# Kernel optimization log

Hardware: AMD Instinct MI355X
Metric: run time of the kernel (lower is better)

Reference implementation:

```python
import jax, jax.numpy as jnp
import numpy as np


def fake_quant(w, bits):
    # Symmetric per-tensor fake quantization with straight-through estimator.
    qmax = 2.0 ** (bits - 1) - 1.0
    scale = jnp.max(jnp.abs(w)) / qmax
    wq = jnp.clip(jnp.round(w / scale), -qmax, qmax) * scale
    return w + jax.lax.stop_gradient(wq - w)


def setup_inputs() -> dict:
    key = jax.random.key(0)
    k = jax.random.split(key, 5)
    B, S, D, H = 64, 196, 768, 3072
    x = jax.random.normal(k[0], (B, S, D), dtype=jnp.float32)
    w1 = jax.random.normal(k[1], (H, D), dtype=jnp.float32) * (1.0 / np.sqrt(D))
    b1 = jax.random.normal(k[2], (H,), dtype=jnp.float32) * 0.01
    w2 = jax.random.normal(k[3], (D, H), dtype=jnp.float32) * (1.0 / np.sqrt(H))
    b2 = jax.random.normal(k[4], (D,), dtype=jnp.float32) * 0.01
    return {"x": x, "w1": w1, "b1": b1, "w2": w2, "b2": b2, "bits": 8}


def reference(x, w1, b1, w2, b2, bits):
    # fc1 (fake-quant weight) -> ReLU -> fc2 (fake-quant weight)
    w1q = fake_quant(w1, bits)
    w2q = fake_quant(w2, bits)
    h = jnp.einsum('bsd,hd->bsh', x, w1q) + b1   # [B,S,3072]
    h = jax.nn.relu(h)
    out = jnp.einsum('bsh,dh->bsd', h, w2q) + b2  # [B,S,768]
    return out
```

## Files before the change

kernel.cpp:

```cpp
#include <hip/hip_runtime.h>
#include <hip/hip_bf16.h>
#include <stdint.h>

typedef __attribute__((ext_vector_type(8))) short bf16x8;
typedef __attribute__((ext_vector_type(4))) float f32x4;

__device__ __forceinline__ unsigned short f2bf(float f) {
  __hip_bfloat16 h = __float2bfloat16(f);
  return *reinterpret_cast<unsigned short*>(&h);
}

__global__ void prep_kernel(const float* __restrict__ w1, const float* __restrict__ w2,
                            const float* __restrict__ x, int n4w, int n4x,
                            unsigned int* __restrict__ pmax,
                            unsigned short* __restrict__ ox) {
  if (blockIdx.y == 2) {
    const float4* x4 = reinterpret_cast<const float4*>(x);
    ushort4* o4 = reinterpret_cast<ushort4*>(ox);
    for (int i = blockIdx.x * blockDim.x + threadIdx.x; i < n4x;
         i += gridDim.x * blockDim.x) {
      float4 v = x4[i];
      o4[i] = make_ushort4(f2bf(v.x), f2bf(v.y), f2bf(v.z), f2bf(v.w));
    }
    return;
  }
  const float* w = blockIdx.y ? w2 : w1;
  __shared__ unsigned int red[256];
  unsigned int m = 0u;
  const uint4* w4 = reinterpret_cast<const uint4*>(w);
  for (int i = blockIdx.x * blockDim.x + threadIdx.x; i < n4w;
       i += gridDim.x * blockDim.x) {
    uint4 v = w4[i];
    m = max(m, v.x & 0x7fffffffu);
    m = max(m, v.y & 0x7fffffffu);
    m = max(m, v.z & 0x7fffffffu);
    m = max(m, v.w & 0x7fffffffu);
  }
  red[threadIdx.x] = m;
  __syncthreads();
  for (int s = 128; s > 0; s >>= 1) {
    if ((int)threadIdx.x < s)
      red[threadIdx.x] = max(red[threadIdx.x], red[threadIdx.x + s]);
    __syncthreads();
  }
  if (threadIdx.x == 0) pmax[blockIdx.y * 512 + blockIdx.x] = red[0];
}

__global__ void quant2_kernel(const float* __restrict__ w1, const float* __restrict__ w2,
                              int n4, const unsigned int* __restrict__ pmax,
                              const int* __restrict__ bits,
                              unsigned short* __restrict__ o1, unsigned short* __restrict__ o2) {
  __shared__ unsigned int red[256];
  const unsigned int* p = pmax + blockIdx.y * 512;
  red[threadIdx.x] = max(p[threadIdx.x], p[threadIdx.x + 256]);
  __syncthreads();
  for (int s = 128; s > 0; s >>= 1) {
    if ((int)threadIdx.x < s)
      red[threadIdx.x] = max(red[threadIdx.x], red[threadIdx.x + s]);
    __syncthreads();
  }
  const float qmax = (float)((1 << (*bits - 1)) - 1);
  const float scale = __uint_as_float(red[0]) / qmax;

  const float* w = blockIdx.y ? w2 : w1;
  unsigned short* o = blockIdx.y ? o2 : o1;
  const float4* w4 = reinterpret_cast<const float4*>(w);
  ushort4* o4 = reinterpret_cast<ushort4*>(o);
  for (int i = blockIdx.x * blockDim.x + threadIdx.x; i < n4;
       i += gridDim.x * blockDim.x) {
    float4 v = w4[i];
    float a = fminf(fmaxf(rintf(v.x / scale), -qmax), qmax) * scale;
    float b = fminf(fmaxf(rintf(v.y / scale), -qmax), qmax) * scale;
    float c = fminf(fmaxf(rintf(v.z / scale), -qmax), qmax) * scale;
    float d = fminf(fmaxf(rintf(v.w / scale), -qmax), qmax) * scale;
    o4[i] = make_ushort4(f2bf(a), f2bf(b), f2bf(c), f2bf(d));
  }
}

template<bool PRIO, bool RELU, bool BF16_OUT>
__global__ __launch_bounds__(256, 4)
void gemm_bt32(const unsigned short* __restrict__ A,
               const unsigned short* __restrict__ B,
               const float* __restrict__ bias,
               void* __restrict__ Cout,
               int M, int N, int K, int gx) {
  constexpr int BK = 32, MF = 4;
  __shared__ __attribute__((aligned(16))) unsigned short As[2][128 * BK];
  __shared__ __attribute__((aligned(16))) unsigned short Bs[2][128 * BK];

  const int nwg = gridDim.x;
  const int orig = blockIdx.x;
  const int q = nwg >> 3, r = nwg & 7;
  const int xcd = orig & 7, cidx = orig >> 3;
  const int wgid = (xcd < r ? xcd * (q + 1) : r * (q + 1) + (xcd - r) * q) + cidx;
  const int bx = wgid % gx;
  const int by = wgid / gx;

  const int tid = threadIdx.x;
  const int lane = tid & 63;
  const int wave = tid >> 6;
  const int wr = wave >> 1;
  const int wc = wave & 1;
  const long brow = (long)by * 128;
  const long bcol = (long)bx * 128;

  f32x4 acc[MF][4] = {};

  const int srow = lane >> 2;
  const int gslot = ((lane & 3) ^ ((lane >> 3) & 3)) * 8;
  const int fr = lane & 15;
  const int fs = lane >> 4;

  auto stage = [&](int k0, int b) {
#pragma unroll
    for (int it = 0; it < 2; ++it) {
      const int c = it * 4 + wave;
      const unsigned short* ga = A + (brow + c * 16 + srow) * (long)K + k0 + gslot;
      __builtin_amdgcn_global_load_lds(
          (const __attribute__((address_space(1))) void*)ga,
          (__attribute__((address_space(3))) void*)(&As[b][c * 512]), 16, 0, 0);
    }
#pragma unroll
    for (int it = 0; it < 2; ++it) {
      const int c = it * 4 + wave;
      const unsigned short* gb = B + (bcol + c * 16 + srow) * (long)K + k0 + gslot;
      __builtin_amdgcn_global_load_lds(
          (const __attribute__((address_space(1))) void*)gb,
          (__attribute__((address_space(3))) void*)(&Bs[b][c * 512]), 16, 0, 0);
    }
  };

  const int nt = K / BK;
  stage(0, 0);
  stage(BK, 1);

  for (int t = 0; t < nt; ++t) {
    const int b = t & 1;
    if (t < nt - 1) asm volatile("s_waitcnt vmcnt(4)" ::: "memory");
    else            asm volatile("s_waitcnt vmcnt(0)" ::: "memory");
    __builtin_amdgcn_s_barrier();

    const unsigned short* as = &As[b][0];
    const unsigned short* bs = &Bs[b][0];
    bf16x8 a[MF], bb[4];
#pragma unroll
    for (int m = 0; m < MF; ++m) {
      const int row = wr * 64 + m * 16 + fr;
      a[m] = *reinterpret_cast<const bf16x8*>(as + row * BK + ((fs ^ ((row >> 1) & 3)) * 8));
    }
#pragma unroll
    for (int n = 0; n < 4; ++n) {
      const int row = wc * 64 + n * 16 + fr;
      bb[n] = *reinterpret_cast<const bf16x8*>(bs + row * BK + ((fs ^ ((row >> 1) & 3)) * 8));
    }
    if (PRIO) __builtin_amdgcn_s_setprio(1);
#pragma unroll
    for (int m = 0; m < MF; ++m)
#pragma unroll
      for (int n = 0; n < 4; ++n)
        acc[m][n] = __builtin_amdgcn_mfma_f32_16x16x32_bf16(a[m], bb[n], acc[m][n], 0, 0, 0);
    if (PRIO) __builtin_amdgcn_s_setprio(0);

    asm volatile("s_waitcnt lgkmcnt(0)" ::: "memory");
    __builtin_amdgcn_sched_barrier(0);
    __builtin_amdgcn_s_barrier();
    if (t + 2 < nt) stage((t + 2) * BK, b);
  }

  const int fq = lane >> 4;
#pragma unroll
  for (int n = 0; n < 4; ++n) {
    const long col = bcol + wc * 64 + n * 16 + fr;
    const float bv = bias[col];
#pragma unroll
    for (int m = 0; m < MF; ++m) {
#pragma unroll
      for (int rr = 0; rr < 4; ++rr) {
        const long row = brow + wr * 64 + m * 16 + fq * 4 + rr;
        float v = acc[m][n][rr] + bv;
        if (RELU) v = fmaxf(v, 0.0f);
        if (BF16_OUT)
          ((unsigned short*)Cout)[row * N + col] = f2bf(v);
        else
          ((float*)Cout)[row * N + col] = v;
      }
    }
  }
}

template<int BM, bool PRIO, bool RELU, bool BF16_OUT>
__global__ __launch_bounds__(256)
void gemm_bt(const unsigned short* __restrict__ A, const unsigned short* __restrict__ B,
             const float* __restrict__ bias, void* __restrict__ Cout,
             int M, int N, int K, int gx) {
  constexpr int BK = 64;
  constexpr int MF = BM / 32;
  __shared__ __attribute__((aligned(16))) unsigned short As[2][BM * BK];
  __shared__ __attribute__((aligned(16))) unsigned short Bs[2][128 * BK];

  const int nwg = gridDim.x;
  const int orig = blockIdx.x;
  const int q = nwg >> 3, r = nwg & 7;
  const int xcd = orig & 7, cidx = orig >> 3;
  const int wgid = (xcd < r ? xcd * (q + 1) : r * (q + 1) + (xcd - r) * q) + cidx;
  const int bx = wgid % gx;
  const int by = wgid / gx;

  const int tid = threadIdx.x;
  const int lane = tid & 63;
  const int wave = tid >> 6;
  const int wr = wave >> 1;
  const int wc = wave & 1;
  const long brow = (long)by * BM;
  const long bcol = (long)bx * 128;

  f32x4 acc[MF][4] = {};

  const int srow = lane >> 3;
  const int gslot = ((lane & 7) ^ (lane >> 3)) * 8;
  const int fr = lane & 15;
  const int fs = lane >> 4;

  auto stage = [&](int k0, int b) {
#pragma unroll
    for (int it = 0; it < BM / 32; ++it) {
      const int c = it * 4 + wave;
      const unsigned short* ga = A + (brow + c * 8 + srow) * (long)K + k0 + gslot;
      __builtin_amdgcn_global_load_lds(
          (const __attribute__((address_space(1))) void*)ga,
          (__attribute__((address_space(3))) void*)(&As[b][c * 512]), 16, 0, 0);
    }
#pragma unroll
    for (int it = 0; it < 4; ++it) {
      const int c = it * 4 + wave;
      const unsigned short* gb = B + (bcol + c * 8 + srow) * (long)K + k0 + gslot;
      __builtin_amdgcn_global_load_lds(
          (const __attribute__((address_space(1))) void*)gb,
          (__attribute__((address_space(3))) void*)(&Bs[b][c * 512]), 16, 0, 0);
    }
  };

  const int nt = K / BK;
  stage(0, 0);
  stage(BK, 1);

  for (int t = 0; t < nt; ++t) {
    const int b = t & 1;
    if (t < nt - 1) {
      if constexpr (BM == 128) asm volatile("s_waitcnt vmcnt(8)" ::: "memory");
      else                     asm volatile("s_waitcnt vmcnt(6)" ::: "memory");
    } else {
      asm volatile("s_waitcnt vmcnt(0)" ::: "memory");
    }
    __builtin_amdgcn_s_barrier();

    const unsigned short* as = &As[b][0];
    const unsigned short* bs = &Bs[b][0];
#pragma unroll
    for (int kk = 0; kk < 2; ++kk) {
      const int s = kk * 4 + fs;
      bf16x8 a[MF], bb[4];
#pragma unroll
      for (int m = 0; m < MF; ++m) {
        const int row = wr * (MF * 16) + m * 16 + fr;
        a[m] = *reinterpret_cast<const bf16x8*>(as + row * BK + ((s ^ (row & 7)) * 8));
      }
#pragma unroll
      for (int n = 0; n < 4; ++n) {
        const int row = wc * 64 + n * 16 + fr;
        bb[n] = *reinterpret_cast<const bf16x8*>(bs + row * BK + ((s ^ (row & 7)) * 8));
      }
      if (PRIO) __builtin_amdgcn_s_setprio(1);
#pragma unroll
      for (int m = 0; m < MF; ++m)
#pragma unroll
        for (int n = 0; n < 4; ++n)
          acc[m][n] = __builtin_amdgcn_mfma_f32_16x16x32_bf16(a[m], bb[n], acc[m][n], 0, 0, 0);
      if (PRIO) __builtin_amdgcn_s_setprio(0);
    }

    asm volatile("s_waitcnt lgkmcnt(0)" ::: "memory");
    __builtin_amdgcn_sched_barrier(0);
    __builtin_amdgcn_s_barrier();
    if (t + 2 < nt) stage((t + 2) * BK, b);
  }

  const int fq = lane >> 4;
#pragma unroll
  for (int n = 0; n < 4; ++n) {
    const long col = bcol + wc * 64 + n * 16 + fr;
    const float bv = bias[col];
#pragma unroll
    for (int m = 0; m < MF; ++m) {
#pragma unroll
      for (int rr = 0; rr < 4; ++rr) {
        const long row = brow + wr * (MF * 16) + m * 16 + fq * 4 + rr;
        float v = acc[m][n][rr] + bv;
        if (RELU) v = fmaxf(v, 0.0f);
        if (BF16_OUT)
          ((unsigned short*)Cout)[row * N + col] = f2bf(v);
        else
          ((float*)Cout)[row * N + col] = v;
      }
    }
  }
}

extern "C" void kernel_launch(void* const* d_in, const int* in_sizes, int n_in,
                              void* d_out, int out_size, void* d_ws, size_t ws_size,
                              hipStream_t stream) {
  const float* x  = (const float*)d_in[0];
  const float* w1 = (const float*)d_in[1];
  const float* b1 = (const float*)d_in[2];
  const float* w2 = (const float*)d_in[3];
  const float* b2 = (const float*)d_in[4];
  const int* bits = (const int*)d_in[5];

  const int M = 64 * 196;
  const int D = 768, H = 3072;
  const int nx = M * D;
  const int nw1 = H * D;

  char* ws = (char*)d_ws;
  unsigned short* xb  = (unsigned short*)(ws + 256);
  unsigned short* w1q = (unsigned short*)(ws + 256 + (size_t)nx * 2);
  unsigned short* w2q = (unsigned short*)(ws + 256 + (size_t)nx * 2 + (size_t)nw1 * 2);
  unsigned short* hb  = (unsigned short*)(ws + 256 + (size_t)nx * 2 + (size_t)nw1 * 4);
  unsigned int* pmax = (unsigned int*)hb;

  prep_kernel<<<dim3(512, 3), 256, 0, stream>>>(w1, w2, x, nw1 / 4, nx / 4, pmax, xb);
  quant2_kernel<<<dim3(512, 2), 256, 0, stream>>>(w1, w2, nw1 / 4, pmax, bits, w1q, w2q);

  gemm_bt32<true, true, true><<<(H / 128) * (M / 128), 256, 0, stream>>>(
      xb, w1q, b1, hb, M, H, D, H / 128);
  gemm_bt<64, true, false, false><<<(D / 128) * (M / 64), 256, 0, stream>>>(
      hb, w2q, b2, d_out, M, D, H, D / 128);
}
```

Before: 184.4 us.

## Fuse weight absmax and quantization into one cooperative kernel with register reuse

Replaces the separate absmax-reduction and quantization kernels with a single cooperative kernel that holds each thread's weight elements in registers across a grid-wide sync. The weights no longer have to be read from global memory twice, and one kernel launch goes away. The x-to-bf16 conversion runs between the two grid syncs to hide the global reduction. The risk is the cost of grid synchronization, the register pressure from keeping 10 uint4 values per thread, and the requirement that all 512 blocks be co-resident.

```diff
diff --git a/kernel.cpp b/kernel.cpp
--- a/kernel.cpp
+++ b/kernel.cpp
@@ -1,5 +1,6 @@
 #include <hip/hip_runtime.h>
 #include <hip/hip_bf16.h>
+#include <hip/hip_cooperative_groups.h>
 #include <stdint.h>
 
 typedef __attribute__((ext_vector_type(8))) short bf16x8;
@@ -10,70 +11,99 @@
   return *reinterpret_cast<unsigned short*>(&h);
 }
 
-__global__ void prep_kernel(const float* __restrict__ w1, const float* __restrict__ w2,
-                            const float* __restrict__ x, int n4w, int n4x,
-                            unsigned int* __restrict__ pmax,
-                            unsigned short* __restrict__ ox) {
-  if (blockIdx.y == 2) {
+__global__ __launch_bounds__(256)
+void prepquant_coop(const float* __restrict__ w1, const float* __restrict__ w2,
+                    const float* __restrict__ x, int n4w, int n4x,
+                    const int* __restrict__ bits,
+                    unsigned int* __restrict__ pmax,
+                    unsigned int* __restrict__ gbits,
+                    unsigned short* __restrict__ o1, unsigned short* __restrict__ o2,
+                    unsigned short* __restrict__ ox) {
+  cooperative_groups::grid_group grid = cooperative_groups::this_grid();
+  const int tid = blockIdx.x * blockDim.x + threadIdx.x;
+  constexpr int NTHR = 512 * 256;
+
+  const uint4* w14 = reinterpret_cast<const uint4*>(w1);
+  const uint4* w24 = reinterpret_cast<const uint4*>(w2);
+  uint4 s1[5], s2[5];
+  unsigned int m1 = 0u, m2 = 0u;
+#pragma unroll
+  for (int k = 0; k < 5; ++k) {
+    const int i = tid + k * NTHR;
+    if (k < 4 || i < n4w) {
+      uint4 v = w14[i];
+      s1[k] = v;
+      m1 = max(m1, max(max(v.x & 0x7fffffffu, v.y & 0x7fffffffu),
+                       max(v.z & 0x7fffffffu, v.w & 0x7fffffffu)));
+      uint4 u = w24[i];
+      s2[k] = u;
+      m2 = max(m2, max(max(u.x & 0x7fffffffu, u.y & 0x7fffffffu),
+                       max(u.z & 0x7fffffffu, u.w & 0x7fffffffu)));
+    }
+  }
+  __shared__ unsigned int red[2][256];
+  red[0][threadIdx.x] = m1;
+  red[1][threadIdx.x] = m2;
+  __syncthreads();
+  for (int s = 128; s > 0; s >>= 1) {
+    if ((int)threadIdx.x < s) {
+      red[0][threadIdx.x] = max(red[0][threadIdx.x], red[0][threadIdx.x + s]);
+      red[1][threadIdx.x] = max(red[1][threadIdx.x], red[1][threadIdx.x + s]);
+    }
+    __syncthreads();
+  }
+  if (threadIdx.x == 0) {
+    pmax[blockIdx.x] = red[0][0];
+    pmax[512 + blockIdx.x] = red[1][0];
+  }
+  __threadfence();
+  grid.sync();
+
+  if (blockIdx.x < 2) {
+    const unsigned int* p = pmax + blockIdx.x * 512;
+    unsigned int mm = max(p[threadIdx.x], p[threadIdx.x + 256]);
+    red[0][threadIdx.x] = mm;
+    __syncthreads();
+    for (int s = 128; s > 0; s >>= 1) {
+      if ((int)threadIdx.x < s)
+        red[0][threadIdx.x] = max(red[0][threadIdx.x], red[0][threadIdx.x + s]);
+      __syncthreads();
+    }
+    if (threadIdx.x == 0) gbits[blockIdx.x] = red[0][0];
+    __threadfence();
+  }
+  {
     const float4* x4 = reinterpret_cast<const float4*>(x);
     ushort4* o4 = reinterpret_cast<ushort4*>(ox);
-    for (int i = blockIdx.x * blockDim.x + threadIdx.x; i < n4x;
-         i += gridDim.x * blockDim.x) {
+    for (int i = tid; i < n4x; i += NTHR) {
       float4 v = x4[i];
       o4[i] = make_ushort4(f2bf(v.x), f2bf(v.y), f2bf(v.z), f2bf(v.w));
     }
-    return;
-  }
-  const float* w = blockIdx.y ? w2 : w1;
-  __shared__ unsigned int red[256];
-  unsigned int m = 0u;
-  const uint4* w4 = reinterpret_cast<const uint4*>(w);
-  for (int i = blockIdx.x * blockDim.x + threadIdx.x; i < n4w;
-       i += gridDim.x * blockDim.x) {
-    uint4 v = w4[i];
-    m = max(m, v.x & 0x7fffffffu);
-    m = max(m, v.y & 0x7fffffffu);
-    m = max(m, v.z & 0x7fffffffu);
-    m = max(m, v.w & 0x7fffffffu);
-  }
-  red[threadIdx.x] = m;
-  __syncthreads();
-  for (int s = 128; s > 0; s >>= 1) {
-    if ((int)threadIdx.x < s)
-      red[threadIdx.x] = max(red[threadIdx.x], red[threadIdx.x + s]);
-    __syncthreads();
-  }
-  if (threadIdx.x == 0) pmax[blockIdx.y * 512 + blockIdx.x] = red[0];
-}
-
-__global__ void quant2_kernel(const float* __restrict__ w1, const float* __restrict__ w2,
-                              int n4, const unsigned int* __restrict__ pmax,
-                              const int* __restrict__ bits,
-                              unsigned short* __restrict__ o1, unsigned short* __restrict__ o2) {
-  __shared__ unsigned int red[256];
-  const unsigned int* p = pmax + blockIdx.y * 512;
-  red[threadIdx.x] = max(p[threadIdx.x], p[threadIdx.x + 256]);
-  __syncthreads();
-  for (int s = 128; s > 0; s >>= 1) {
-    if ((int)threadIdx.x < s)
-      red[threadIdx.x] = max(red[threadIdx.x], red[threadIdx.x + s]);
-    __syncthreads();
-  }
+  }
+  grid.sync();
+
   const float qmax = (float)((1 << (*bits - 1)) - 1);
-  const float scale = __uint_as_float(red[0]) / qmax;
-
-  const float* w = blockIdx.y ? w2 : w1;
-  unsigned short* o = blockIdx.y ? o2 : o1;
-  const float4* w4 = reinterpret_cast<const float4*>(w);
-  ushort4* o4 = reinterpret_cast<ushort4*>(o);
-  for (int i = blockIdx.x * blockDim.x + threadIdx.x; i < n4;
-       i += gridDim.x * blockDim.x) {
-    float4 v = w4[i];
-    float a = fminf(fmaxf(rintf(v.x / scale), -qmax), qmax) * scale;
-    float b = fminf(fmaxf(rintf(v.y / scale), -qmax), qmax) * scale;
-    float c = fminf(fmaxf(rintf(v.z / scale), -qmax), qmax) * scale;
-    float d = fminf(fmaxf(rintf(v.w / scale), -qmax), qmax) * scale;
-    o4[i] = make_ushort4(f2bf(a), f2bf(b), f2bf(c), f2bf(d));
+  const float sc1 = __uint_as_float(gbits[0]) / qmax;
+  const float sc2 = __uint_as_float(gbits[1]) / qmax;
+  ushort4* o14 = reinterpret_cast<ushort4*>(o1);
+  ushort4* o24 = reinterpret_cast<ushort4*>(o2);
+#pragma unroll
+  for (int k = 0; k < 5; ++k) {
+    const int i = tid + k * NTHR;
+    if (k < 4 || i < n4w) {
+      float4 v = *reinterpret_cast<float4*>(&s1[k]);
+      o14[i] = make_ushort4(
+          f2bf(fminf(fmaxf(rintf(v.x / sc1), -qmax), qmax) * sc1),
+          f2bf(fminf(fmaxf(rintf(v.y / sc1), -qmax), qmax) * sc1),
+          f2bf(fminf(fmaxf(rintf(v.z / sc1), -qmax), qmax) * sc1),
+          f2bf(fminf(fmaxf(rintf(v.w / sc1), -qmax), qmax) * sc1));
+      float4 u = *reinterpret_cast<float4*>(&s2[k]);
+      o24[i] = make_ushort4(
+          f2bf(fminf(fmaxf(rintf(u.x / sc2), -qmax), qmax) * sc2),
+          f2bf(fminf(fmaxf(rintf(u.y / sc2), -qmax), qmax) * sc2),
+          f2bf(fminf(fmaxf(rintf(u.z / sc2), -qmax), qmax) * sc2),
+          f2bf(fminf(fmaxf(rintf(u.w / sc2), -qmax), qmax) * sc2));
+    }
   }
 }
 
@@ -322,14 +352,19 @@
   const int nw1 = H * D;
 
   char* ws = (char*)d_ws;
-  unsigned short* xb  = (unsigned short*)(ws + 256);
-  unsigned short* w1q = (unsigned short*)(ws + 256 + (size_t)nx * 2);
-  unsigned short* w2q = (unsigned short*)(ws + 256 + (size_t)nx * 2 + (size_t)nw1 * 2);
-  unsigned short* hb  = (unsigned short*)(ws + 256 + (size_t)nx * 2 + (size_t)nw1 * 4);
-  unsigned int* pmax = (unsigned int*)hb;
-
-  prep_kernel<<<dim3(512, 3), 256, 0, stream>>>(w1, w2, x, nw1 / 4, nx / 4, pmax, xb);
-  quant2_kernel<<<dim3(512, 2), 256, 0, stream>>>(w1, w2, nw1 / 4, pmax, bits, w1q, w2q);
+  unsigned int* pmax  = (unsigned int*)ws;
+  unsigned int* gbits = (unsigned int*)(ws + 8192);
+  unsigned short* xb  = (unsigned short*)(ws + 16384);
+  unsigned short* w1q = (unsigned short*)(ws + 16384 + (size_t)nx * 2);
+  unsigned short* w2q = (unsigned short*)(ws + 16384 + (size_t)nx * 2 + (size_t)nw1 * 2);
+  unsigned short* hb  = (unsigned short*)(ws + 16384 + (size_t)nx * 2 + (size_t)nw1 * 4);
+
+  int n4w = nw1 / 4, n4x = nx / 4;
+  void* args[] = {(void*)&w1, (void*)&w2, (void*)&x, (void*)&n4w, (void*)&n4x,
+                  (void*)&bits, (void*)&pmax, (void*)&gbits,
+                  (void*)&w1q, (void*)&w2q, (void*)&xb};
+  hipLaunchCooperativeKernel((const void*)prepquant_coop, dim3(512), dim3(256),
+                             args, 0, stream);
 
   gemm_bt32<true, true, true><<<(H / 128) * (M / 128), 256, 0, stream>>>(
       xb, w1q, b1, hb, M, H, D, H / 128);
```

New measurement: 307.0 us. 1.67x slower.
